# Optimization experiments

Hardware: AMD Instinct MI355X
Metric: run time of the kernel (lower is better)

## Reference

```python
import jax, jax.numpy as jnp
import numpy as np

B, Q, V, T = 96, 96, 197, 77   # image batch, text batch, visual tokens, text tokens
DV, DT, E = 768, 768, 512      # visual_size, textual_size, embed_size


def l2norm(x):
    # F.normalize(t, dim=-1, p=2) with eps=1e-12
    n = jnp.linalg.norm(x, axis=-1, keepdims=True)
    return x / jnp.maximum(n, 1e-12)


def setup_inputs() -> dict:
    key = jax.random.key(0)
    ks = jax.random.split(key, 12)
    sv = 1.0 / np.sqrt(DV).astype(np.float32)
    st = 1.0 / np.sqrt(DT).astype(np.float32)
    return {
        "visual_cls": jax.random.normal(ks[0], (B, DV), jnp.float32),
        "visual_tokens": jax.random.normal(ks[1], (B, V, DV), jnp.float32),
        "textual_cls": jax.random.normal(ks[2], (Q, DT), jnp.float32),
        "textual_tokens": jax.random.normal(ks[3], (Q, T, DT), jnp.float32),
        "Wv_cls": jax.random.normal(ks[4], (E, DV), jnp.float32) * sv,
        "bv_cls": jnp.zeros((E,), jnp.float32),
        "Wt_cls": jax.random.normal(ks[5], (E, DT), jnp.float32) * st,
        "bt_cls": jnp.zeros((E,), jnp.float32),
        "Wv_tok": jax.random.normal(ks[6], (E, DV), jnp.float32) * sv,
        "bv_tok": jnp.zeros((E,), jnp.float32),
        "Wt_tok": jax.random.normal(ks[7], (E, DT), jnp.float32) * st,
        "bt_tok": jnp.zeros((E,), jnp.float32),
        "text_length": jax.random.randint(ks[8], (Q,), 5, T + 1, jnp.int32),
    }


def reference(visual_cls, visual_tokens, textual_cls, textual_tokens,
              Wv_cls, bv_cls, Wt_cls, bt_cls,
              Wv_tok, bv_tok, Wt_tok, bt_tok, text_length):
    # Linear projections (torch nn.Linear: y = x @ W.T + b)
    v_cls = visual_cls @ Wv_cls.T + bv_cls            # [b, e]
    t_cls = textual_cls @ Wt_cls.T + bt_cls           # [q, e]
    v_tok = l2norm(jnp.einsum('bvd,ed->bve', visual_tokens, Wv_tok) + bv_tok)   # [b, v, e]
    t_tok = l2norm(jnp.einsum('qtd,ed->qte', textual_tokens, Wt_tok) + bt_tok)  # [q, t, e]

    # valid-token mask from caption lengths: mask[q, t]
    mask = (jnp.arange(T)[None, :] < text_length[:, None]).astype(v_tok.dtype)

    # fine-grained token similarity: [b, q, v, t], masked on text tokens
    logits = jnp.einsum('bve,qte->bqvt', v_tok, t_tok) * mask[None, :, None, :]

    text_sum = mask.sum(-1)                           # [q]
    t2v = logits.max(axis=2).sum(axis=2) / text_sum[None, :]   # [b, q]
    v2t = logits.max(axis=3).sum(axis=2) / V                   # [b, q]
    return (v_cls, t_cls, t2v, v2t)
```

## Files before the change

### kernel.cpp

```cpp
#include <hip/hip_runtime.h>

#define NB 96
#define NQ 96
#define NV 197
#define NT 77
#define DK 768
#define DE 512

typedef __attribute__((ext_vector_type(8))) short s16x8;
typedef __attribute__((ext_vector_type(4))) float f32x4;
typedef long long i64;

__device__ __forceinline__ unsigned short f2bf(float f) {
  union { float f; unsigned int u; } v; v.f = f;
  unsigned int u = v.u;
  unsigned int r = u + 0x7fffu + ((u >> 16) & 1u);
  return (unsigned short)(r >> 16);
}

__device__ __forceinline__ unsigned int pack2bf(float a, float b) {
  return (unsigned int)f2bf(a) | ((unsigned int)f2bf(b) << 16);
}

__device__ __forceinline__ unsigned char f2fp8(float x) {
  union { float f; unsigned u; } v; v.f = x;
  unsigned s = (v.u >> 24) & 0x80;
  v.u &= 0x7FFFFFFFu;
  if (v.f < 0.015625f) {
    int q = __float2int_rn(v.f * 512.0f);
    return (unsigned char)(s | (unsigned)q);
  }
  if (v.f >= 464.0f) return (unsigned char)(s | 0x7E);
  int e8 = (int)((v.u >> 23) & 0xFF) - 120;
  unsigned m = v.u & 0x7FFFFFu;
  unsigned t = ((unsigned)e8 << 3) | (m >> 20);
  unsigned r = m & 0xFFFFFu;
  t += (r > 0x80000u) || ((r == 0x80000u) && (t & 1u));
  if (t > 0x7Eu) t = 0x7Eu;
  return (unsigned char)(s | t);
}

#define GL16(gp, lp, off)                                                \
  __builtin_amdgcn_global_load_lds(                                      \
      (const __attribute__((address_space(1))) void*)(gp),               \
      (__attribute__((address_space(3))) void*)(lp), 16, (off), 0)

#define VM_DRAIN() asm volatile("s_waitcnt vmcnt(0) lgkmcnt(0)" ::: "memory")

__global__ __launch_bounds__(256) void prep_kernel(
    const float* __restrict__ Wv_tok, unsigned short* __restrict__ Wvb,
    const float* __restrict__ Wt_tok, unsigned short* __restrict__ Wtb,
    const float* __restrict__ visual_cls, const float* __restrict__ Wv_cls,
    const float* __restrict__ bv_cls, float* __restrict__ v_cls_o,
    const float* __restrict__ textual_cls, const float* __restrict__ Wt_cls,
    const float* __restrict__ bt_cls, float* __restrict__ t_cls_o) {
  __shared__ float xs[DK];
  const int blk = blockIdx.x;
  const int tid = threadIdx.x;

  if (blk < 768) {
    const float* src = (blk < 384) ? Wv_tok : Wt_tok;
    unsigned short* dst = (blk < 384) ? Wvb : Wtb;
    int i = ((blk < 384) ? blk : (blk - 384)) * 256 + tid;
    float4 x = ((const float4*)src)[i];
    ushort4 h;
    h.x = f2bf(x.x); h.y = f2bf(x.y); h.z = f2bf(x.z); h.w = f2bf(x.w);
    ((ushort4*)dst)[i] = h;
    return;
  }
  const int is_t = (blk >= 864);
  const int row = blk - (is_t ? 864 : 768);
  const float* X = is_t ? textual_cls : visual_cls;
  const float* W = is_t ? Wt_cls : Wv_cls;
  const float* bias = is_t ? bt_cls : bv_cls;
  float* out = is_t ? t_cls_o : v_cls_o;

  const float* xr = X + (long)row * DK;
  for (int i = tid; i < DK; i += 256) xs[i] = xr[i];
  __syncthreads();
  for (int c = tid; c < DE; c += 256) {
    const float* wr = W + (long)c * DK;
    float s = 0.f;
    #pragma unroll 4
    for (int k = 0; k < DK; k += 4) {
      float4 w4 = *(const float4*)(wr + k);
      s += xs[k] * w4.x + xs[k + 1] * w4.y + xs[k + 2] * w4.z + xs[k + 3] * w4.w;
    }
    out[(long)row * DE + c] = s + bias[c];
  }
}

__global__ __launch_bounds__(256, 2) void proj_norm_kernel(
    const float* __restrict__ Xv, const unsigned short* __restrict__ Wvb,
    const float* __restrict__ bv, unsigned char* __restrict__ Yv,
    const float* __restrict__ Xt, const unsigned short* __restrict__ Wtb,
    const float* __restrict__ bt, unsigned char* __restrict__ Yt) {
  __shared__ __align__(16) unsigned short Ws[512 * 64];
  __shared__ __align__(16) unsigned short Xs[64 * 64];
  __shared__ float ssq_lds[4][64];

  const int blk = blockIdx.x;
  const int is_t = (blk >= 296);
  const float* X = is_t ? Xt : Xv;
  const unsigned short* Wb = is_t ? Wtb : Wvb;
  const float* bias = is_t ? bt : bv;
  unsigned char* Y = is_t ? Yt : Yv;
  const int M = is_t ? (NQ * NT) : (NB * NV);
  const long row0 = (long)(is_t ? (blk - 296) : blk) * 64;

  const int tid = threadIdx.x;
  const int wave = tid >> 6;
  const int lane = tid & 63;
  const int l15 = lane & 15;
  const int quad = lane >> 4;

  const int sub = lane >> 3;
  const int swz = ((lane & 7) ^ sub) << 3;
  const unsigned short* pw_base = Wb + (long)(wave * 8 + sub) * DK + swz;

  const int xrow_a = tid >> 3;
  const int xrow_b = xrow_a + 32;
  const int xs8 = tid & 7;
  long gra = row0 + xrow_a; if (gra > M - 1) gra = M - 1;
  long grb = row0 + xrow_b; if (grb > M - 1) grb = M - 1;
  const float* px_a = X + gra * DK + xs8 * 8;
  const float* px_b = X + grb * DK + xs8 * 8;
  const int xaddr_a = (xrow_a << 6) + ((xs8 ^ (xrow_a & 7)) << 3);
  const int xaddr_b = (xrow_b << 6) + ((xs8 ^ (xrow_b & 7)) << 3);

  f32x4 acc[4][8];
  #pragma unroll
  for (int m = 0; m < 4; ++m)
    #pragma unroll
    for (int n = 0; n < 8; ++n)
      acc[m][n] = (f32x4){0.f, 0.f, 0.f, 0.f};

  for (int kc = 0; kc < DK; kc += 64) {
    __syncthreads();
    {
      float4 x0 = *(const float4*)(px_a);
      float4 x1 = *(const float4*)(px_a + 4);
      uint4 h;
      h.x = pack2bf(x0.x, x0.y); h.y = pack2bf(x0.z, x0.w);
      h.z = pack2bf(x1.x, x1.y); h.w = pack2bf(x1.z, x1.w);
      *(uint4*)(&Xs[xaddr_a]) = h;
      x0 = *(const float4*)(px_b);
      x1 = *(const float4*)(px_b + 4);
      h.x = pack2bf(x0.x, x0.y); h.y = pack2bf(x0.z, x0.w);
      h.z = pack2bf(x1.x, x1.y); h.w = pack2bf(x1.z, x1.w);
      *(uint4*)(&Xs[xaddr_b]) = h;
      px_a += 64; px_b += 64;
    }
    {
      const unsigned short* pw = pw_base;
      #pragma unroll
      for (int j = 0; j < 16; ++j) {
        GL16(pw, &Ws[(j * 4 + wave) << 9], 0);
        pw += 32 * DK;
      }
      pw_base += 64;
    }
    VM_DRAIN();
    __syncthreads();
    #pragma unroll
    for (int ks = 0; ks < 2; ++ks) {
      s16x8 af[4];
      #pragma unroll
      for (int mi = 0; mi < 4; ++mi) {
        int arow = mi * 16 + l15;
        af[mi] = *(const s16x8*)&Xs[(arow << 6) + ((((ks << 2) + quad) ^ (arow & 7)) << 3)];
      }
      #pragma unroll
      for (int nt = 0; nt < 8; ++nt) {
        int wrow = wave * 128 + nt * 16 + l15;
        s16x8 bfr = *(const s16x8*)&Ws[(wrow << 6) + ((((ks << 2) + quad) ^ (wrow & 7)) << 3)];
        #pragma unroll
        for (int mi = 0; mi < 4; ++mi)
          acc[mi][nt] = __builtin_amdgcn_mfma_f32_16x16x32_bf16(af[mi], bfr, acc[mi][nt], 0, 0, 0);
      }
    }
  }

  #pragma unroll
  for (int nt = 0; nt < 8; ++nt) {
    float bc = bias[wave * 128 + nt * 16 + l15];
    #pragma unroll
    for (int mi = 0; mi < 4; ++mi) {
      acc[mi][nt].x += bc; acc[mi][nt].y += bc; acc[mi][nt].z += bc; acc[mi][nt].w += bc;
    }
  }

  #pragma unroll
  for (int mi = 0; mi < 4; ++mi)
    #pragma unroll
    for (int r = 0; r < 4; ++r) {
      float t = 0.f;
      #pragma unroll
      for (int nt = 0; nt < 8; ++nt) { float v = acc[mi][nt][r]; t += v * v; }
      t += __shfl_xor(t, 1);
      t += __shfl_xor(t, 2);
      t += __shfl_xor(t, 4);
      t += __shfl_xor(t, 8);
      if (l15 == 0) ssq_lds[wave][mi * 16 + quad * 4 + r] = t;
    }
  __syncthreads();

  #pragma unroll
  for (int mi = 0; mi < 4; ++mi) {
    #pragma unroll
    for (int r = 0; r < 4; ++r) {
      int rr = mi * 16 + quad * 4 + r;
      float tot = ssq_lds[0][rr] + ssq_lds[1][rr] + ssq_lds[2][rr] + ssq_lds[3][rr];
      float scale = (tot > 0.f) ? (1.f / fmaxf(sqrtf(tot), 1e-12f)) : 0.f;
      long grow = row0 + rr;
      if (grow < M) {
        #pragma unroll
        for (int nt = 0; nt < 8; ++nt) {
          int col = wave * 128 + nt * 16 + l15;
          Y[grow * DE + col] = f2fp8(acc[mi][nt][r] * scale);
        }
      }
    }
  }
}

__global__ __launch_bounds__(256, 2) void score_kernel(
    const unsigned char* __restrict__ Yv, const unsigned char* __restrict__ Yt,
    const int* __restrict__ tlen, float* __restrict__ t2v, float* __restrict__ v2t) {
  __shared__ __align__(16) unsigned char As[2][104 * 128];
  __shared__ __align__(16) unsigned char Bs[2][80 * 128];
  __shared__ float colbuf[4][160];
  __shared__ float rowsum_lds[4][2];

  const int tid = threadIdx.x;
  const int wave = tid >> 6;
  const int lane = tid & 63;
  const int l15 = lane & 15;
  const int quad = lane >> 4;

  const int idx = blockIdx.x;
  const int x = idx & 7;
  const int g = idx >> 3;
  const int qi = g / 12;
  const int bslot = g - qi * 12;
  const int b = bslot * 8 + x;
  const int q0 = qi * 2;

  const unsigned char* Ab = Yv + (long)b * (NV * DE);
  const unsigned char* Bb = Yt + (long)q0 * (NT * DE);

  {
    unsigned int* za = (unsigned int*)&As[0][0];
    for (int i = tid; i < 6656; i += 256) za[i] = 0;
    unsigned int* zb = (unsigned int*)&Bs[0][0];
    for (int i = tid; i < 5120; i += 256) zb[i] = 0;
  }
  __syncthreads();

  const int ul = lane >> 3;
  const int slot = lane & 7;
  const int kq16 = (((slot >> 1) ^ (ul & 3)) << 4);

  auto a_ptr = [&](int s) -> const unsigned char* {
    int row = (s * 8 + ul) * 2 + (slot & 1);
    if (row > NV - 1) row = NV - 1;
    return Ab + row * DE + kq16;
  };
  auto b_ptr = [&](int s) -> const unsigned char* {
    int r = (s * 8 + ul) * 2 + (slot & 1);
    int half = (r >= 80) ? 1 : 0;
    int t = r - 80 * half;
    if (t > NT - 1) t = NT - 1;
    return Bb + (long)half * (NT * DE) + t * DE + kq16;
  };

  const unsigned char* sp0 = a_ptr(wave);
  const unsigned char* sp1 = a_ptr(wave + 4);
  const unsigned char* sp2 = a_ptr(wave + 8);
  const int s3 = (wave == 1) ? 8 : (wave == 2) ? 9 : 12;
  const int b3_is_b = (wave == 1 || wave == 2);
  const unsigned char* sp3 = b3_is_b ? b_ptr(s3) : a_ptr(12);
  const unsigned char* sp4 = b_ptr(wave);
  const unsigned char* sp5 = b_ptr(wave + 4);
  unsigned char* b3d0 = b3_is_b ? &Bs[0][s3 << 10] : &As[0][12 << 10];
  unsigned char* b3d1 = b3_is_b ? &Bs[1][s3 << 10] : &As[1][12 << 10];

  const int qh = quad >> 1;
  const int q8 = (quad & 1) << 3;
  int aoff[4], boff[10];
  #pragma unroll
  for (int i = 0; i < 4; ++i) {
    int arow = (wave + i * 4) * 16 + l15;
    int u = arow >> 1;
    aoff[i] = (u << 7) + (((qh ^ (u & 3))) << 5) + ((arow & 1) << 4) + q8;
  }
  #pragma unroll
  for (int nt = 0; nt < 10; ++nt) {
    int brow = nt * 16 + l15;
    int u = brow >> 1;
    boff[nt] = (u << 7) + (((qh ^ (u & 3))) << 5) + ((brow & 1) << 4) + q8;
  }

  f32x4 acc[4][10];
  #pragma unroll
  for (int i = 0; i < 4; ++i)
    #pragma unroll
    for (int nt = 0; nt < 10; ++nt)
      acc[i][nt] = (f32x4){0.f, 0.f, 0.f, 0.f};

  auto do_compute = [&](int p) {
    #pragma unroll
    for (int ks = 0; ks < 2; ++ks) {
      const int kx = ks ? 64 : 0;
      i64 bf[10];
      #pragma unroll
      for (int nt = 0; nt < 10; ++nt)
        bf[nt] = *(const i64*)&Bs[p][boff[nt] ^ kx];
      __builtin_amdgcn_s_setprio(1);
      #pragma unroll
      for (int i = 0; i < 4; ++i) {
        int mt = wave + (i << 2);
        if (mt < 13) {
          i64 af = *(const i64*)&As[p][aoff[i] ^ kx];
          #pragma unroll
          for (int nt = 0; nt < 10; ++nt)
            acc[i][nt] = __builtin_amdgcn_mfma_f32_16x16x32_fp8_fp8(af, bf[nt], acc[i][nt], 0, 0, 0);
        }
      }
      __builtin_amdgcn_s_setprio(0);
    }
  };

#define SCORE_STAGE(p, b3p)                                              \
  {                                                                      \
    GL16(sp0, &As[p][(wave) << 10], 0);                                  \
    GL16(sp1, &As[p][(wave + 4) << 10], 0);                              \
    GL16(sp2, &As[p][(wave + 8) << 10], 0);                              \
    GL16(sp3, (b3p), 0);                                                 \
    GL16(sp4, &Bs[p][(wave) << 10], 0);                                  \
    GL16(sp5, &Bs[p][(wave + 4) << 10], 0);                              \
    sp0 += 64; sp1 += 64; sp2 += 64; sp3 += 64; sp4 += 64; sp5 += 64;    \
  }

#define SCORE_ITER(cur, b3p, do_stage)                                   \
  {                                                                      \
    asm volatile("s_waitcnt vmcnt(0)" ::: "memory");                     \
    __syncthreads();                                                     \
    if (do_stage) SCORE_STAGE(1 - (cur), b3p);                           \
    do_compute(cur);                                                     \
  }

  SCORE_STAGE(0, b3d0)
  SCORE_ITER(0, b3d1, 1)
  SCORE_ITER(1, b3d0, 1)
  SCORE_ITER(0, b3d1, 1)
  SCORE_ITER(1, b3d0, 1)
  SCORE_ITER(0, b3d1, 1)
  SCORE_ITER(1, b3d0, 1)
  SCORE_ITER(0, b3d1, 1)
  SCORE_ITER(1, b3d0, 0)

#undef SCORE_ITER
#undef SCORE_STAGE

  const int len0 = tlen[q0];
  const int len1 = tlen[q0 + 1];

  #pragma unroll
  for (int nt = 0; nt < 10; ++nt) {
    float m = -1e30f;
    #pragma unroll
    for (int i = 0; i < 4; ++i) {
      int mt = wave + (i << 2);
      if (mt < 13) {
        int mbase = mt * 16 + quad * 4;
        #pragma unroll
        for (int r = 0; r < 4; ++r)
          if (mbase + r < NV) m = fmaxf(m, acc[i][nt][r]);
      }
    }
    m = fmaxf(m, __shfl_xor(m, 16));
    m = fmaxf(m, __shfl_xor(m, 32));
    if (lane < 16) colbuf[wave][nt * 16 + l15] = m;
  }

  float psum[2] = {0.f, 0.f};
  #pragma unroll
  for (int h = 0; h < 2; ++h) {
    int len = h ? len1 : len0;
    #pragma unroll
    for (int i = 0; i < 4; ++i) {
      int mt = wave + (i << 2);
      if (mt < 13) {
        int mbase = mt * 16 + quad * 4;
        #pragma unroll
        for (int r = 0; r < 4; ++r) {
          float rm = -1e30f;
          #pragma unroll
          for (int nt = 0; nt < 5; ++nt) {
            int c = nt * 16 + l15;
            if (c < len) rm = fmaxf(rm, acc[i][h * 5 + nt][r]);
          }
          rm = fmaxf(rm, __shfl_xor(rm, 1));
          rm = fmaxf(rm, __shfl_xor(rm, 2));
          rm = fmaxf(rm, __shfl_xor(rm, 4));
          rm = fmaxf(rm, __shfl_xor(rm, 8));
          if (len < NT) rm = fmaxf(rm, 0.f);
          if (l15 == 0 && (mbase + r) < NV) psum[h] += rm;
        }
      }
    }
    psum[h] += __shfl_xor(psum[h], 16);
    psum[h] += __shfl_xor(psum[h], 32);
  }
  if (lane == 0) { rowsum_lds[wave][0] = psum[0]; rowsum_lds[wave][1] = psum[1]; }
  __syncthreads();

  if (wave < 2) {
    int q = q0 + wave;
    int len = wave ? len1 : len0;
    int cbase = wave * 80;
    float ssum = 0.f;
    for (int c = lane; c < 80; c += 64) {
      if (c < len) {
        float m = fmaxf(fmaxf(colbuf[0][cbase + c], colbuf[1][cbase + c]),
                        fmaxf(colbuf[2][cbase + c], colbuf[3][cbase + c]));
        ssum += m;
      }
    }
    ssum += __shfl_xor(ssum, 1);
    ssum += __shfl_xor(ssum, 2);
    ssum += __shfl_xor(ssum, 4);
    ssum += __shfl_xor(ssum, 8);
    ssum += __shfl_xor(ssum, 16);
    ssum += __shfl_xor(ssum, 32);
    if (lane == 0) {
      float rs = rowsum_lds[0][wave] + rowsum_lds[1][wave] +
                 rowsum_lds[2][wave] + rowsum_lds[3][wave];
      t2v[b * NQ + q] = ssum / (float)len;
      v2t[b * NQ + q] = rs / (float)NV;
    }
  }
}

extern "C" void kernel_launch(void* const* d_in, const int* in_sizes, int n_in,
                              void* d_out, int out_size, void* d_ws, size_t ws_size,
                              hipStream_t stream) {
  (void)in_sizes; (void)n_in; (void)out_size; (void)ws_size;
  const float* visual_cls     = (const float*)d_in[0];
  const float* visual_tokens  = (const float*)d_in[1];
  const float* textual_cls    = (const float*)d_in[2];
  const float* textual_tokens = (const float*)d_in[3];
  const float* Wv_cls = (const float*)d_in[4];
  const float* bv_cls = (const float*)d_in[5];
  const float* Wt_cls = (const float*)d_in[6];
  const float* bt_cls = (const float*)d_in[7];
  const float* Wv_tok = (const float*)d_in[8];
  const float* bv_tok = (const float*)d_in[9];
  const float* Wt_tok = (const float*)d_in[10];
  const float* bt_tok = (const float*)d_in[11];
  const int* text_length = (const int*)d_in[12];

  float* out = (float*)d_out;
  float* v_cls_o = out;
  float* t_cls_o = out + 49152;
  float* t2v_o   = out + 98304;
  float* v2t_o   = out + 107520;

  char* ws = (char*)d_ws;
  unsigned short* Wvb = (unsigned short*)(ws);
  unsigned short* Wtb = (unsigned short*)(ws + 786432);
  unsigned char*  Yv  = (unsigned char*)(ws + 1572864);
  unsigned char*  Yt  = (unsigned char*)(ws + 1572864 + 9683968);

  prep_kernel<<<960, 256, 0, stream>>>(
      Wv_tok, Wvb, Wt_tok, Wtb,
      visual_cls, Wv_cls, bv_cls, v_cls_o,
      textual_cls, Wt_cls, bt_cls, t_cls_o);

  proj_norm_kernel<<<412, 256, 0, stream>>>(
      visual_tokens, Wvb, bv_tok, Yv,
      textual_tokens, Wtb, bt_tok, Yt);

  score_kernel<<<(NB * NQ) / 2, 256, 0, stream>>>(Yv, Yt, text_length, t2v_o, v2t_o);
}
```

Measured before the change: 416.7 us.

## Preload whole text tile into LDS and stream visual fragments directly to registers

The score kernel now loads the full K extent of the two-caption text tile into one LDS pool up front, packing the two captions contiguously (154 rows instead of two padded 80-row halves). The visual A operand is no longer staged through LDS; each lane loads its fp8 MFMA fragments straight from global memory into registers, double-buffered across K chunks. This drops the per-iteration vmcnt drains, barriers and LDS zeroing of the old double-buffered pipeline. In exchange LDS use grows to about 79 KB per block, which may limit occupancy, and A reads become uncoalesced 8-byte accesses. The epilogue column indexing is adjusted to match the packed layout.

Result: faster. 405.0 us (-2.8%).

```diff
diff --git a/kernel.cpp b/kernel.cpp
--- a/kernel.cpp
+++ b/kernel.cpp
@@ -227,10 +227,9 @@
 __global__ __launch_bounds__(256, 2) void score_kernel(
     const unsigned char* __restrict__ Yv, const unsigned char* __restrict__ Yt,
     const int* __restrict__ tlen, float* __restrict__ t2v, float* __restrict__ v2t) {
-  __shared__ __align__(16) unsigned char As[2][104 * 128];
-  __shared__ __align__(16) unsigned char Bs[2][80 * 128];
-  __shared__ float colbuf[4][160];
-  __shared__ float rowsum_lds[4][2];
+  __shared__ __align__(16) unsigned char pool[79232];
+  float (*colbuf)[160] = (float(*)[160])pool;
+  float (*rowsum_lds)[2] = (float(*)[2])(pool + 2560);
 
   const int tid = threadIdx.x;
   const int wave = tid >> 6;
@@ -249,56 +248,42 @@
   const unsigned char* Ab = Yv + (long)b * (NV * DE);
   const unsigned char* Bb = Yt + (long)q0 * (NT * DE);
 
-  {
-    unsigned int* za = (unsigned int*)&As[0][0];
-    for (int i = tid; i < 6656; i += 256) za[i] = 0;
-    unsigned int* zb = (unsigned int*)&Bs[0][0];
-    for (int i = tid; i < 5120; i += 256) zb[i] = 0;
-  }
-  __syncthreads();
+  if (tid < 96) *(int*)(pool + 78848 + tid * 4) = 0;
+
+  const unsigned char* pa[4];
+  #pragma unroll
+  for (int i = 0; i < 4; ++i) {
+    int row = (wave + (i << 2)) * 16 + l15;
+    if (row > NV - 1) row = NV - 1;
+    pa[i] = Ab + row * DE + (quad << 3);
+  }
 
   const int ul = lane >> 3;
   const int slot = lane & 7;
-  const int kq16 = (((slot >> 1) ^ (ul & 3)) << 4);
-
-  auto a_ptr = [&](int s) -> const unsigned char* {
-    int row = (s * 8 + ul) * 2 + (slot & 1);
-    if (row > NV - 1) row = NV - 1;
-    return Ab + row * DE + kq16;
-  };
-  auto b_ptr = [&](int s) -> const unsigned char* {
-    int r = (s * 8 + ul) * 2 + (slot & 1);
-    int half = (r >= 80) ? 1 : 0;
-    int t = r - 80 * half;
-    if (t > NT - 1) t = NT - 1;
-    return Bb + (long)half * (NT * DE) + t * DE + kq16;
-  };
-
-  const unsigned char* sp0 = a_ptr(wave);
-  const unsigned char* sp1 = a_ptr(wave + 4);
-  const unsigned char* sp2 = a_ptr(wave + 8);
-  const int s3 = (wave == 1) ? 8 : (wave == 2) ? 9 : 12;
-  const int b3_is_b = (wave == 1 || wave == 2);
-  const unsigned char* sp3 = b3_is_b ? b_ptr(s3) : a_ptr(12);
-  const unsigned char* sp4 = b_ptr(wave);
-  const unsigned char* sp5 = b_ptr(wave + 4);
-  unsigned char* b3d0 = b3_is_b ? &Bs[0][s3 << 10] : &As[0][12 << 10];
-  unsigned char* b3d1 = b3_is_b ? &Bs[1][s3 << 10] : &As[1][12 << 10];
+  #pragma unroll
+  for (int cc = 0; cc < 2; ++cc) {
+    const int c = wave * 2 + cc;
+    const unsigned char* cb = Bb + c * 64;
+    #pragma unroll
+    for (int s = 0; s < 10; ++s) {
+      int u = (s < 9) ? (s * 8 + ul) : (69 + ul);
+      int r = u * 2 + (slot & 1);
+      int h = (r >= NT);
+      int t = r - NT * h;
+      const unsigned char* gp = cb + ((long)h * NT + t) * DE + (((slot >> 1) ^ (u & 3)) << 4);
+      int sbase = (s < 9) ? (s << 10) : 8832;
+      GL16(gp, pool + c * 9856 + sbase, 0);
+    }
+  }
 
   const int qh = quad >> 1;
   const int q8 = (quad & 1) << 3;
-  int aoff[4], boff[10];
-  #pragma unroll
-  for (int i = 0; i < 4; ++i) {
-    int arow = (wave + i * 4) * 16 + l15;
-    int u = arow >> 1;
-    aoff[i] = (u << 7) + (((qh ^ (u & 3))) << 5) + ((arow & 1) << 4) + q8;
-  }
+  int boff[10];
   #pragma unroll
   for (int nt = 0; nt < 10; ++nt) {
     int brow = nt * 16 + l15;
     int u = brow >> 1;
-    boff[nt] = (u << 7) + (((qh ^ (u & 3))) << 5) + ((brow & 1) << 4) + q8;
+    boff[nt] = (u << 7) + ((qh ^ (u & 3)) << 5) + ((brow & 1) << 4) + q8;
   }
 
   f32x4 acc[4][10];
@@ -308,60 +293,59 @@
     for (int nt = 0; nt < 10; ++nt)
       acc[i][nt] = (f32x4){0.f, 0.f, 0.f, 0.f};
 
-  auto do_compute = [&](int p) {
+  auto do_compute = [&](int c, const i64* af) {
+    const int base = c * 9856;
     #pragma unroll
     for (int ks = 0; ks < 2; ++ks) {
       const int kx = ks ? 64 : 0;
       i64 bf[10];
       #pragma unroll
       for (int nt = 0; nt < 10; ++nt)
-        bf[nt] = *(const i64*)&Bs[p][boff[nt] ^ kx];
+        bf[nt] = *(const i64*)&pool[base + (boff[nt] ^ kx)];
       __builtin_amdgcn_s_setprio(1);
       #pragma unroll
       for (int i = 0; i < 4; ++i) {
-        int mt = wave + (i << 2);
-        if (mt < 13) {
-          i64 af = *(const i64*)&As[p][aoff[i] ^ kx];
+        if (wave + (i << 2) < 13) {
           #pragma unroll
           for (int nt = 0; nt < 10; ++nt)
-            acc[i][nt] = __builtin_amdgcn_mfma_f32_16x16x32_fp8_fp8(af, bf[nt], acc[i][nt], 0, 0, 0);
+            acc[i][nt] = __builtin_amdgcn_mfma_f32_16x16x32_fp8_fp8(
+                af[i * 2 + ks], bf[nt], acc[i][nt], 0, 0, 0);
         }
       }
       __builtin_amdgcn_s_setprio(0);
     }
   };
 
-#define SCORE_STAGE(p, b3p)                                              \
+#define LOADA(c, af)                                                     \
   {                                                                      \
-    GL16(sp0, &As[p][(wave) << 10], 0);                                  \
-    GL16(sp1, &As[p][(wave + 4) << 10], 0);                              \
-    GL16(sp2, &As[p][(wave + 8) << 10], 0);                              \
-    GL16(sp3, (b3p), 0);                                                 \
-    GL16(sp4, &Bs[p][(wave) << 10], 0);                                  \
-    GL16(sp5, &Bs[p][(wave + 4) << 10], 0);                              \
-    sp0 += 64; sp1 += 64; sp2 += 64; sp3 += 64; sp4 += 64; sp5 += 64;    \
-  }
-
-#define SCORE_ITER(cur, b3p, do_stage)                                   \
-  {                                                                      \
-    asm volatile("s_waitcnt vmcnt(0)" ::: "memory");                     \
-    __syncthreads();                                                     \
-    if (do_stage) SCORE_STAGE(1 - (cur), b3p);                           \
-    do_compute(cur);                                                     \
-  }
-
-  SCORE_STAGE(0, b3d0)
-  SCORE_ITER(0, b3d1, 1)
-  SCORE_ITER(1, b3d0, 1)
-  SCORE_ITER(0, b3d1, 1)
-  SCORE_ITER(1, b3d0, 1)
-  SCORE_ITER(0, b3d1, 1)
-  SCORE_ITER(1, b3d0, 1)
-  SCORE_ITER(0, b3d1, 1)
-  SCORE_ITER(1, b3d0, 0)
-
-#undef SCORE_ITER
-#undef SCORE_STAGE
+    _Pragma("unroll")                                                    \
+    for (int i = 0; i < 4; ++i) {                                        \
+      if (wave + (i << 2) < 13) {                                        \
+        af[i * 2]     = *(const i64*)(pa[i] + (c) * 64);                 \
+        af[i * 2 + 1] = *(const i64*)(pa[i] + (c) * 64 + 32);            \
+      }                                                                  \
+    }                                                                    \
+  }
+
+  i64 af0[8] = {0, 0, 0, 0, 0, 0, 0, 0};
+  i64 af1[8] = {0, 0, 0, 0, 0, 0, 0, 0};
+
+  LOADA(0, af0)
+  VM_DRAIN();
+  __syncthreads();
+
+  LOADA(1, af1)  do_compute(0, af0);
+  LOADA(2, af0)  do_compute(1, af1);
+  LOADA(3, af1)  do_compute(2, af0);
+  LOADA(4, af0)  do_compute(3, af1);
+  LOADA(5, af1)  do_compute(4, af0);
+  LOADA(6, af0)  do_compute(5, af1);
+  LOADA(7, af1)  do_compute(6, af0);
+  do_compute(7, af1);
+
+#undef LOADA
+
+  __syncthreads();
 
   const int len0 = tlen[q0];
   const int len1 = tlen[q0 + 1];
@@ -386,42 +370,52 @@
 
   float psum[2] = {0.f, 0.f};
   #pragma unroll
-  for (int h = 0; h < 2; ++h) {
-    int len = h ? len1 : len0;
-    #pragma unroll
-    for (int i = 0; i < 4; ++i) {
-      int mt = wave + (i << 2);
-      if (mt < 13) {
-        int mbase = mt * 16 + quad * 4;
+  for (int i = 0; i < 4; ++i) {
+    int mt = wave + (i << 2);
+    if (mt < 13) {
+      int mbase = mt * 16 + quad * 4;
+      #pragma unroll
+      for (int r = 0; r < 4; ++r) {
+        float rm = -1e30f;
         #pragma unroll
-        for (int r = 0; r < 4; ++r) {
-          float rm = -1e30f;
-          #pragma unroll
-          for (int nt = 0; nt < 5; ++nt) {
-            int c = nt * 16 + l15;
-            if (c < len) rm = fmaxf(rm, acc[i][h * 5 + nt][r]);
-          }
-          rm = fmaxf(rm, __shfl_xor(rm, 1));
-          rm = fmaxf(rm, __shfl_xor(rm, 2));
-          rm = fmaxf(rm, __shfl_xor(rm, 4));
-          rm = fmaxf(rm, __shfl_xor(rm, 8));
-          if (len < NT) rm = fmaxf(rm, 0.f);
-          if (l15 == 0 && (mbase + r) < NV) psum[h] += rm;
+        for (int nt = 0; nt < 5; ++nt) {
+          int gcol = nt * 16 + l15;
+          if (gcol < len0) rm = fmaxf(rm, acc[i][nt][r]);
         }
-      }
-    }
-    psum[h] += __shfl_xor(psum[h], 16);
-    psum[h] += __shfl_xor(psum[h], 32);
-  }
+        rm = fmaxf(rm, __shfl_xor(rm, 1));
+        rm = fmaxf(rm, __shfl_xor(rm, 2));
+        rm = fmaxf(rm, __shfl_xor(rm, 4));
+        rm = fmaxf(rm, __shfl_xor(rm, 8));
+        if (len0 < NT) rm = fmaxf(rm, 0.f);
+        if (l15 == 0 && (mbase + r) < NV) psum[0] += rm;
+        float rm1 = -1e30f;
+        #pragma unroll
+        for (int nt = 4; nt < 10; ++nt) {
+          int gcol = nt * 16 + l15;
+          if (gcol >= NT && gcol < NT + len1) rm1 = fmaxf(rm1, acc[i][nt][r]);
+        }
+        rm1 = fmaxf(rm1, __shfl_xor(rm1, 1));
+        rm1 = fmaxf(rm1, __shfl_xor(rm1, 2));
+        rm1 = fmaxf(rm1, __shfl_xor(rm1, 4));
+        rm1 = fmaxf(rm1, __shfl_xor(rm1, 8));
+        if (len1 < NT) rm1 = fmaxf(rm1, 0.f);
+        if (l15 == 0 && (mbase + r) < NV) psum[1] += rm1;
+      }
+    }
+  }
+  psum[0] += __shfl_xor(psum[0], 16);
+  psum[0] += __shfl_xor(psum[0], 32);
+  psum[1] += __shfl_xor(psum[1], 16);
+  psum[1] += __shfl_xor(psum[1], 32);
   if (lane == 0) { rowsum_lds[wave][0] = psum[0]; rowsum_lds[wave][1] = psum[1]; }
   __syncthreads();
 
   if (wave < 2) {
     int q = q0 + wave;
     int len = wave ? len1 : len0;
-    int cbase = wave * 80;
+    int cbase = wave * NT;
     float ssum = 0.f;
-    for (int c = lane; c < 80; c += 64) {
+    for (int c = lane; c < NT; c += 64) {
       if (c < len) {
         float m = fmaxf(fmaxf(colbuf[0][cbase + c], colbuf[1][cbase + c]),
                         fmaxf(colbuf[2][cbase + c], colbuf[3][cbase + c]));
```
